# Performance work log

Measured on AMD Instinct MI355X. Metric: run time of the kernel, lower is better.

The kernel has to match this reference:

```python
import jax, jax.numpy as jnp
import numpy as np

EPS = 1e-8           # torch.cosine_similarity norm clamp
TEMPERATURE = 0.2    # from __init__ default


def setup_inputs() -> dict:
    key = jax.random.key(0)
    k1, k2, k3 = jax.random.split(key, 3)
    B, C, D = 16384, 1000, 2048  # batch, num_classes, embedding_size
    querys = jax.random.normal(k1, (B, D), dtype=jnp.float32)
    prototype = jax.random.normal(k2, (C, D), dtype=jnp.float32)
    fc_w = jax.random.normal(k3, (C, D), dtype=jnp.float32) * 0.02
    fc_b = jnp.zeros((C,), dtype=jnp.float32)
    return {"querys": querys, "prototype": prototype, "fc_w": fc_w, "fc_b": fc_b}


def _memory_prototype_attention(querys, prototype):
    # cosine similarity of every query against every prototype, fused as one GEMM
    qn = jnp.maximum(jnp.linalg.norm(querys, axis=1, keepdims=True), EPS)      # [B,1]
    pn = jnp.maximum(jnp.linalg.norm(prototype, axis=1, keepdims=True), EPS)   # [C,1]
    cos = jnp.einsum('bd,cd->bc', querys / qn, prototype / pn)                 # [B,C]
    attn = jax.nn.softmax(cos / TEMPERATURE, axis=1)                           # [B,C]
    enhanced = jnp.einsum('bc,cd->bd', attn, prototype)                        # [B,D]
    # original skips rows where the raw score sum is exactly zero
    nonzero = (jnp.sum(cos, axis=1, keepdims=True) != 0)
    return jnp.where(nonzero, enhanced, jnp.zeros_like(enhanced))


def reference(querys, prototype, fc_w, fc_b):
    embedding = querys  # post-avgpool features in the original forward
    enhanced = jax.lax.stop_gradient(_memory_prototype_attention(querys, prototype))
    x = querys + enhanced
    logits = x @ fc_w.T + fc_b  # [B, num_classes]
    return (logits, embedding)
```

## Files before the change

kernel.cpp:

```cpp
#include <hip/hip_runtime.h>
#include <hip/hip_bf16.h>
#include <cstdint>
#include <math.h>

typedef __attribute__((ext_vector_type(8))) __bf16 bfx8;
typedef __attribute__((ext_vector_type(4))) __bf16 bfx4;
typedef __attribute__((ext_vector_type(4))) float f32x4;

#define EPSN 1e-8f
#define SM_SCALE 7.2134752044448170f

__device__ __forceinline__ void gload_lds16(const void* g, void* l) {
    __builtin_amdgcn_global_load_lds(
        (__attribute__((address_space(1))) void*)g,
        (__attribute__((address_space(3))) void*)l,
        16, 0, 0);
}

__global__ __launch_bounds__(256) void qnorm_kernel(
    const float* __restrict__ q, __bf16* __restrict__ qbf,
    float* __restrict__ emb, int D) {
    const int tid = threadIdx.x;
    const size_t roff = (size_t)blockIdx.x * D;
    const float4* qr = (const float4*)(q + roff);
    float4* er = (float4*)(emb + roff);
    const int PASS = D >> 10;
    float4 v[4];
    float ss = 0.f;
    for (int p = 0; p < PASS; ++p) {
        v[p] = qr[p * 256 + tid];
        ss += v[p].x * v[p].x + v[p].y * v[p].y + v[p].z * v[p].z + v[p].w * v[p].w;
    }
    for (int o = 32; o; o >>= 1) ss += __shfl_xor(ss, o);
    __shared__ float sred[4];
    if ((tid & 63) == 0) sred[tid >> 6] = ss;
    __syncthreads();
    float tot = sred[0] + sred[1] + sred[2] + sred[3];
    float inv = 1.f / fmaxf(sqrtf(tot), EPSN);
    for (int p = 0; p < PASS; ++p) {
        er[p * 256 + tid] = v[p];
        bfx4 o4 = {(__bf16)(v[p].x * inv), (__bf16)(v[p].y * inv),
                   (__bf16)(v[p].z * inv), (__bf16)(v[p].w * inv)};
        *(bfx4*)(qbf + roff + (size_t)(p * 256 + tid) * 4) = o4;
    }
}

__global__ __launch_bounds__(256) void pnorm_kernel(
    const float* __restrict__ P, const float* __restrict__ W,
    __bf16* __restrict__ Pn, __bf16* __restrict__ Wb,
    int C, int D) {
    const int c = blockIdx.x;
    const int tid = threadIdx.x;
    const int PASS = D >> 10;
    if (c >= C) {
        bfx4 z = {(__bf16)0.f, (__bf16)0.f, (__bf16)0.f, (__bf16)0.f};
        for (int p = 0; p < PASS; ++p) {
            size_t e = (size_t)c * D + (size_t)(p * 256 + tid) * 4;
            *(bfx4*)(Pn + e) = z;
            *(bfx4*)(Wb + e) = z;
        }
        return;
    }
    const float4* pr = (const float4*)(P + (size_t)c * D);
    float4 v[4];
    float ss = 0.f;
    for (int p = 0; p < PASS; ++p) {
        v[p] = pr[p * 256 + tid];
        ss += v[p].x * v[p].x + v[p].y * v[p].y + v[p].z * v[p].z + v[p].w * v[p].w;
    }
    for (int o = 32; o; o >>= 1) ss += __shfl_xor(ss, o);
    __shared__ float sred[4];
    if ((tid & 63) == 0) sred[tid >> 6] = ss;
    __syncthreads();
    float tot = sred[0] + sred[1] + sred[2] + sred[3];
    float inv = 1.f / fmaxf(sqrtf(tot), EPSN);
    const float4* wr_ = (const float4*)(W + (size_t)c * D);
    for (int p = 0; p < PASS; ++p) {
        size_t e = (size_t)c * D + (size_t)(p * 256 + tid) * 4;
        bfx4 o4 = {(__bf16)(v[p].x * inv), (__bf16)(v[p].y * inv),
                   (__bf16)(v[p].z * inv), (__bf16)(v[p].w * inv)};
        *(bfx4*)(Pn + e) = o4;
        float4 wv = wr_[p * 256 + tid];
        bfx4 w4 = {(__bf16)wv.x, (__bf16)wv.y, (__bf16)wv.z, (__bf16)wv.w};
        *(bfx4*)(Wb + e) = w4;
    }
}

__global__ __launch_bounds__(256) void ptrans_kernel(
    const float* __restrict__ P, __bf16* __restrict__ PT,
    int C, int D, int CP) {
    __shared__ float t[64][65];
    const int d0 = blockIdx.x * 64;
    const int c0 = blockIdx.y * 64;
    const int tid = threadIdx.x;
#pragma unroll
    for (int it = 0; it < 16; ++it) {
        int idx = it * 256 + tid;
        int r = idx >> 6;
        int cc = idx & 63;
        float v = 0.f;
        if (c0 + r < C) v = P[(size_t)(c0 + r) * D + d0 + cc];
        t[r][cc] = v;
    }
    __syncthreads();
#pragma unroll
    for (int it = 0; it < 16; ++it) {
        int idx = it * 256 + tid;
        int dd = idx >> 6;
        int c = idx & 63;
        PT[(size_t)(d0 + dd) * CP + c0 + c] = (__bf16)t[c][dd];
    }
}

__global__ __launch_bounds__(256) void softmax_kernel(
    __bf16* __restrict__ S, int C, int CP) {
    const int tid = threadIdx.x;
    __bf16* row = S + (size_t)blockIdx.x * CP;
    bfx4 v4 = *(const bfx4*)(row + tid * 4);
    const int base = tid * 4;
    float v[4];
    float mx = -INFINITY, rs = 0.f;
#pragma unroll
    for (int j = 0; j < 4; ++j) {
        v[j] = (float)v4[j];
        if (base + j < C) { mx = fmaxf(mx, v[j]); rs += v[j]; }
    }
    for (int o = 32; o; o >>= 1) {
        mx = fmaxf(mx, __shfl_xor(mx, o));
        rs += __shfl_xor(rs, o);
    }
    __shared__ float smx[4], srs[4], sps[4];
    if ((tid & 63) == 0) { smx[tid >> 6] = mx; srs[tid >> 6] = rs; }
    __syncthreads();
    mx = fmaxf(fmaxf(smx[0], smx[1]), fmaxf(smx[2], smx[3]));
    rs = srs[0] + srs[1] + srs[2] + srs[3];
    float p[4], ps = 0.f;
#pragma unroll
    for (int j = 0; j < 4; ++j) {
        p[j] = (base + j < C) ? exp2f((v[j] - mx) * SM_SCALE) : 0.f;
        ps += p[j];
    }
    for (int o = 32; o; o >>= 1) ps += __shfl_xor(ps, o);
    if ((tid & 63) == 0) sps[tid >> 6] = ps;
    __syncthreads();
    ps = sps[0] + sps[1] + sps[2] + sps[3];
    float inv = (rs != 0.f) ? 1.f / ps : 0.f;
    bfx4 o4 = {(__bf16)(p[0] * inv), (__bf16)(p[1] * inv),
               (__bf16)(p[2] * inv), (__bf16)(p[3] * inv)};
    *(bfx4*)(row + tid * 4) = o4;
}

template <int MODE>
__global__ __launch_bounds__(512, 2) void gemm8p(
    const __bf16* __restrict__ A, const __bf16* __restrict__ B_,
    int K, int NT, int nbxl, int nwg,
    void* __restrict__ out, const float* __restrict__ aux, int ldout) {
    __shared__ __bf16 lds[65536];

    const int tid = threadIdx.x;
    const int lane = tid & 63, wid = tid >> 6;
    const int wr = wid >> 2, wc = wid & 3;
    const int fr = lane & 15, fq = lane >> 4;
    const int wr4 = wr * 4, wc2 = wc * 2;
    const int frs = fr * 32 + ((fq * 8) ^ ((fr & 8) << 1));

    const int nbx = 1 << nbxl;
    const int lin = blockIdx.y * nbx + blockIdx.x;
    const int swz = (lin & 7) * (nwg >> 3) + (lin >> 3);
    const int bm0 = (swz >> nbxl) * 256;
    const int bn0 = (swz & (nbx - 1)) * 256;

    int row0, col0, row1, col1;
    {
        int Le = tid * 8;
        int st = Le >> 9, w = Le & 511;
        row0 = (st >> 1) * 16 + (w >> 5);
        col0 = (st & 1) * 32 + ((w & 31) ^ ((w >> 4) & 16));
        Le = tid * 8 + 4096;
        st = Le >> 9; w = Le & 511;
        row1 = (st >> 1) * 16 + (w >> 5);
        col1 = (st & 1) * 32 + ((w & 31) ^ ((w >> 4) & 16));
    }
    const __bf16* Ap = A + (size_t)bm0 * K;
    const __bf16* Bp = B_ + (size_t)bn0 * K;

    auto STAGE = [&](int s) {
        const int t = s >> 2, h = s & 3;
        const int kt = t << 6;
        const int be = ((t & 1) << 14) + ((h >> 1) << 13);
        const __bf16* src = (h & 1) ? Bp : Ap;
        src += (size_t)((h >> 1) * 128) * K + kt;
        __bf16* d = (h & 1) ? (lds + 32768 + be) : (lds + be);
        gload_lds16(src + (size_t)row0 * K + col0, d + tid * 8);
        gload_lds16(src + (size_t)row1 * K + col1, d + tid * 8 + 4096);
    };

    bfx8 fA0[4][2], fA1[4][2], fB0[2][2], fB1[2][2];
    f32x4 acc[4][4][2] = {};

#define RDA(F, H, BUFE) do {                                                   \
    _Pragma("unroll") for (int m_ = 0; m_ < 4; ++m_)                           \
      _Pragma("unroll") for (int ks_ = 0; ks_ < 2; ++ks_)                      \
        F[m_][ks_] = *(const bfx8*)&lds[(BUFE) +                               \
            (((((H) * 8) + wr4 + m_) * 2 + ks_) << 9) + frs];                  \
} while (0)
#define RDB(F, H, BUFE) do {                                                   \
    _Pragma("unroll") for (int n_ = 0; n_ < 2; ++n_)                           \
      _Pragma("unroll") for (int ks_ = 0; ks_ < 2; ++ks_)                      \
        F[n_][ks_] = *(const bfx8*)&lds[32768 + (BUFE) +                       \
            (((((H) * 8) + wc2 + n_) * 2 + ks_) << 9) + frs];                  \
} while (0)
#define MM(QI, FA, FB) do {                                                    \
    __builtin_amdgcn_s_setprio(1);                                             \
    _Pragma("unroll") for (int ks_ = 0; ks_ < 2; ++ks_)                        \
      _Pragma("unroll") for (int m_ = 0; m_ < 4; ++m_)                         \
        _Pragma("unroll") for (int n_ = 0; n_ < 2; ++n_)                       \
          acc[QI][m_][n_] = __builtin_amdgcn_mfma_f32_16x16x32_bf16(           \
              FA[m_][ks_], FB[n_][ks_], acc[QI][m_][n_], 0, 0, 0);             \
    __builtin_amdgcn_s_setprio(0);                                             \
} while (0)
#define BAR __builtin_amdgcn_s_barrier()
#define LGKM(N) asm volatile("s_waitcnt lgkmcnt(" #N ")" ::: "memory")
#define VMC(N) asm volatile("s_waitcnt vmcnt(" #N ")" ::: "memory")

#pragma unroll
    for (int s = 0; s < 6; ++s) STAGE(s);
    VMC(4);
    BAR;
    RDA(fA0, 0, 0);
    RDB(fB0, 0, 0);

    for (int T = 0; T <= NT - 3; ++T) {
        const int bufe = (T & 1) << 14, nbufe = bufe ^ 16384;
        RDB(fB1, 1, bufe); STAGE(4 * T + 6); BAR; LGKM(4);
        MM(0, fA0, fB0); BAR;
        RDA(fA1, 1, bufe); STAGE(4 * T + 7); BAR; LGKM(8);
        MM(1, fA0, fB1); VMC(6); BAR;
        RDA(fA0, 0, nbufe); STAGE(4 * T + 8); BAR; LGKM(8);
        MM(3, fA1, fB1); VMC(6); BAR;
        STAGE(4 * T + 9); BAR; LGKM(8);
        MM(2, fA1, fB0); RDB(fB0, 0, nbufe); VMC(4); BAR;
    }
    {
        const int T = NT - 2;
        const int bufe = (T & 1) << 14, nbufe = bufe ^ 16384;
        RDB(fB1, 1, bufe); STAGE(4 * T + 6); BAR; LGKM(4);
        MM(0, fA0, fB0); BAR;
        RDA(fA1, 1, bufe); STAGE(4 * T + 7); BAR; LGKM(8);
        MM(1, fA0, fB1); VMC(6); BAR;
        RDA(fA0, 0, nbufe); BAR; LGKM(8);
        MM(3, fA1, fB1); VMC(4); BAR;
        BAR; LGKM(8);
        MM(2, fA1, fB0); RDB(fB0, 0, nbufe); VMC(0); BAR;
    }
    {
        const int T = NT - 1;
        const int bufe = (T & 1) << 14;
        RDB(fB1, 1, bufe); BAR; LGKM(4);
        MM(0, fA0, fB0); BAR;
        RDA(fA1, 1, bufe); BAR; LGKM(8);
        MM(1, fA0, fB1); BAR;
        BAR; LGKM(0);
        MM(3, fA1, fB1); BAR;
        MM(2, fA1, fB0);
    }
#undef RDA
#undef RDB
#undef MM
#undef BAR
#undef LGKM
#undef VMC

#pragma unroll
    for (int q = 0; q < 4; ++q) {
        const int qm_ = q >> 1, qn_ = q & 1;
#pragma unroll
        for (int m = 0; m < 4; ++m) {
            const int grb = bm0 + qm_ * 128 + wr * 64 + m * 16 + fq * 4;
#pragma unroll
            for (int n = 0; n < 2; ++n) {
                const int gc = bn0 + qn_ * 128 + wc * 32 + n * 16 + fr;
#pragma unroll
                for (int j = 0; j < 4; ++j) {
                    const int gr = grb + j;
                    const float va = acc[q][m][n][j];
                    if (MODE == 0) {
                        ((__bf16*)out)[(size_t)gr * ldout + gc] = (__bf16)va;
                    } else if (MODE == 1) {
                        ((__bf16*)out)[(size_t)gr * ldout + gc] =
                            (__bf16)(va + aux[(size_t)gr * ldout + gc]);
                    } else {
                        if (gc < ldout)
                            ((float*)out)[(size_t)gr * ldout + gc] = va + aux[gc];
                    }
                }
            }
        }
    }
}

extern "C" void kernel_launch(void* const* d_in, const int* in_sizes, int n_in,
                              void* d_out, int out_size, void* d_ws, size_t ws_size,
                              hipStream_t stream) {
    const float* q  = (const float*)d_in[0];
    const float* pr = (const float*)d_in[1];
    const float* fw = (const float*)d_in[2];
    const float* fb = (const float*)d_in[3];
    const int C = in_sizes[3];
    const int D = in_sizes[1] / C;
    const int B = in_sizes[0] / D;
    const int CP = (C + 127) & ~127;

    float* logits = (float*)d_out;
    float* emb = logits + (size_t)B * C;

    char* w = (char*)d_ws;
    __bf16* Qb = (__bf16*)w; w += (size_t)B * D * 2;
    __bf16* Pn = (__bf16*)w; w += (size_t)CP * D * 2;
    __bf16* PT = (__bf16*)w; w += (size_t)D * CP * 2;
    __bf16* Wb = (__bf16*)w; w += (size_t)CP * D * 2;
    __bf16* Sb = (__bf16*)w; w += (size_t)B * CP * 2;
    __bf16* Xb = Qb;

    qnorm_kernel<<<B, 256, 0, stream>>>(q, Qb, emb, D);
    pnorm_kernel<<<CP, 256, 0, stream>>>(pr, fw, Pn, Wb, C, D);
    ptrans_kernel<<<dim3(D / 64, CP / 64), 256, 0, stream>>>(pr, PT, C, D, CP);

    {
        const int nbx = CP / 256, nby = B / 256;
        gemm8p<0><<<dim3(nbx, nby), 512, 0, stream>>>(
            Qb, Pn, D, D / 64, 2, nbx * nby, (void*)Sb, nullptr, CP);
    }
    softmax_kernel<<<B, 256, 0, stream>>>(Sb, C, CP);
    {
        const int nbx = D / 256, nby = B / 256;
        gemm8p<1><<<dim3(nbx, nby), 512, 0, stream>>>(
            Sb, PT, CP, CP / 64, 3, nbx * nby, (void*)Xb, q, D);
    }
    {
        const int nbx = CP / 256, nby = B / 256;
        gemm8p<2><<<dim3(nbx, nby), 512, 0, stream>>>(
            Xb, Wb, D, D / 64, 2, nbx * nby, (void*)logits, fb, C);
    }
}
```

Before: 387.1 us.

## Precompute GEMM load addresses and reorder LDS fragment prefetch schedule

Replaces the generic STAGE lambda with a macro that reuses precomputed per-thread source pointers, so the address arithmetic in the main loop shrinks. It also reschedules the pipelined GEMM loop: the next tile's A/B fragment reads now happen after the final MFMA group instead of being interleaved, and the vmcnt/lgkmcnt waits change. The aim is less scalar/VALU overhead and a simpler wait pattern. The cost is less overlap between LDS reads and MFMAs, and a risk of hazards if the waits are now mismatched.

Result: no change. 383.5 us (-0.9%).

```diff
diff --git a/kernel.cpp b/kernel.cpp
--- a/kernel.cpp
+++ b/kernel.cpp
@@ -183,17 +183,24 @@
     }
     const __bf16* Ap = A + (size_t)bm0 * K;
     const __bf16* Bp = B_ + (size_t)bn0 * K;
-
-    auto STAGE = [&](int s) {
-        const int t = s >> 2, h = s & 3;
-        const int kt = t << 6;
-        const int be = ((t & 1) << 14) + ((h >> 1) << 13);
-        const __bf16* src = (h & 1) ? Bp : Ap;
-        src += (size_t)((h >> 1) * 128) * K + kt;
-        __bf16* d = (h & 1) ? (lds + 32768 + be) : (lds + be);
-        gload_lds16(src + (size_t)row0 * K + col0, d + tid * 8);
-        gload_lds16(src + (size_t)row1 * K + col1, d + tid * 8 + 4096);
-    };
+    const size_t hstride = (size_t)128 * K;
+    const __bf16* srcA0 = Ap + (size_t)row0 * K + col0;
+    const __bf16* srcA1 = Ap + (size_t)row1 * K + col1;
+    const __bf16* srcB0 = Bp + (size_t)row0 * K + col0;
+    const __bf16* srcB1 = Bp + (size_t)row1 * K + col1;
+    const int ldsoff = tid * 8;
+
+#define STG(H, t) do {                                                         \
+    const int kt_ = (t) << 6;                                                  \
+    __bf16* d_ = lds + ((((t) & 1) << 14) + (((H) >> 1) << 13) +               \
+                        (((H) & 1) ? 32768 : 0)) + ldsoff;                     \
+    const __bf16* s0_ = (((H) & 1) ? srcB0 : srcA0) +                          \
+                        (((H) >> 1) ? hstride : 0) + kt_;                      \
+    const __bf16* s1_ = (((H) & 1) ? srcB1 : srcA1) +                          \
+                        (((H) >> 1) ? hstride : 0) + kt_;                      \
+    gload_lds16(s0_, d_);                                                      \
+    gload_lds16(s1_, d_ + 4096);                                               \
+} while (0)
 
     bfx8 fA0[4][2], fA1[4][2], fB0[2][2], fB1[2][2];
     f32x4 acc[4][4][2] = {};
@@ -223,8 +230,8 @@
 #define LGKM(N) asm volatile("s_waitcnt lgkmcnt(" #N ")" ::: "memory")
 #define VMC(N) asm volatile("s_waitcnt vmcnt(" #N ")" ::: "memory")
 
-#pragma unroll
-    for (int s = 0; s < 6; ++s) STAGE(s);
+    STG(0, 0); STG(1, 0); STG(2, 0); STG(3, 0);
+    STG(0, 1); STG(1, 1);
     VMC(4);
     BAR;
     RDA(fA0, 0, 0);
@@ -232,30 +239,31 @@
 
     for (int T = 0; T <= NT - 3; ++T) {
         const int bufe = (T & 1) << 14, nbufe = bufe ^ 16384;
-        RDB(fB1, 1, bufe); STAGE(4 * T + 6); BAR; LGKM(4);
+        RDB(fB1, 1, bufe); STG(2, T + 1); BAR; LGKM(4);
         MM(0, fA0, fB0); BAR;
-        RDA(fA1, 1, bufe); STAGE(4 * T + 7); BAR; LGKM(8);
-        MM(1, fA0, fB1); VMC(6); BAR;
-        RDA(fA0, 0, nbufe); STAGE(4 * T + 8); BAR; LGKM(8);
-        MM(3, fA1, fB1); VMC(6); BAR;
-        STAGE(4 * T + 9); BAR; LGKM(8);
-        MM(2, fA1, fB0); RDB(fB0, 0, nbufe); VMC(4); BAR;
+        RDA(fA1, 1, bufe); STG(3, T + 1); BAR; LGKM(8);
+        MM(1, fA0, fB1); BAR;
+        STG(0, T + 2); BAR; LGKM(0);
+        MM(3, fA1, fB1); BAR;
+        STG(1, T + 2); BAR;
+        MM(2, fA1, fB0); VMC(4); BAR;
+        RDA(fA0, 0, nbufe); RDB(fB0, 0, nbufe);
     }
     {
         const int T = NT - 2;
         const int bufe = (T & 1) << 14, nbufe = bufe ^ 16384;
-        RDB(fB1, 1, bufe); STAGE(4 * T + 6); BAR; LGKM(4);
+        RDB(fB1, 1, bufe); STG(2, T + 1); BAR; LGKM(4);
         MM(0, fA0, fB0); BAR;
-        RDA(fA1, 1, bufe); STAGE(4 * T + 7); BAR; LGKM(8);
-        MM(1, fA0, fB1); VMC(6); BAR;
-        RDA(fA0, 0, nbufe); BAR; LGKM(8);
-        MM(3, fA1, fB1); VMC(4); BAR;
-        BAR; LGKM(8);
-        MM(2, fA1, fB0); RDB(fB0, 0, nbufe); VMC(0); BAR;
-    }
-    {
-        const int T = NT - 1;
-        const int bufe = (T & 1) << 14;
+        RDA(fA1, 1, bufe); STG(3, T + 1); BAR; LGKM(8);
+        MM(1, fA0, fB1); BAR;
+        BAR; LGKM(0);
+        MM(3, fA1, fB1); BAR;
+        BAR;
+        MM(2, fA1, fB0); VMC(0); BAR;
+        RDA(fA0, 0, nbufe); RDB(fB0, 0, nbufe);
+    }
+    {
+        const int bufe = ((NT - 1) & 1) << 14;
         RDB(fB1, 1, bufe); BAR; LGKM(4);
         MM(0, fA0, fB0); BAR;
         RDA(fA1, 1, bufe); BAR; LGKM(8);
@@ -264,6 +272,7 @@
         MM(3, fA1, fB1); BAR;
         MM(2, fA1, fB0);
     }
+#undef STG
 #undef RDA
 #undef RDB
 #undef MM
```
